# Kernel tuning notes

Hardware: AMD Instinct MI355X
Metric: run time of the kernel (lower is better)

## Reference

```python
import jax, jax.numpy as jnp
import numpy as np

EMB_SIZE = 256  # VQ embedding_size
BETA = 0.25     # commitment cost


def _mlp(x, W1, b1, W2, b2, W3, b3):
    h = jax.nn.relu(x @ W1 + b1)
    h = jax.nn.relu(h @ W2 + b2)
    return h @ W3 + b3


def setup_inputs() -> dict:
    key = jax.random.key(0)
    ks = jax.random.split(key, 5)
    B, D = 1024, 1024
    s = 1.0 / np.sqrt(D)
    return {
        "observation": jax.random.normal(ks[0], (B, D), jnp.float32),
        "W1": jax.random.normal(ks[1], (D, D), jnp.float32) * s,
        "b1": jnp.zeros((D,), jnp.float32),
        "W2": jax.random.normal(ks[2], (D, D), jnp.float32) * s,
        "b2": jnp.zeros((D,), jnp.float32),
        "W3": jax.random.normal(ks[3], (D, D), jnp.float32) * s,
        "b3": jnp.zeros((D,), jnp.float32),
        "codebook": jax.random.normal(ks[4], (512, EMB_SIZE), jnp.float32),
    }


def reference(observation, W1, b1, W2, b2, W3, b3, codebook):
    # Dense encoder
    features = _mlp(observation, W1, b1, W2, b2, W3, b3)  # [B, 1024]
    # Flatten features into embedding_size-dim tokens: [B*4, 256]
    z = features.reshape(-1, EMB_SIZE)
    # Squared euclidean distances to codebook: [N, K]
    d = (jnp.sum(z * z, axis=1, keepdims=True)
         - 2.0 * (z @ codebook.T)
         + jnp.sum(codebook * codebook, axis=1)[None, :])
    idx = jnp.argmin(d, axis=1)                   # [N] nearest code indices
    quantized = codebook[idx]                     # [N, 256] gather
    # VQ losses
    commitment_loss = jnp.mean((jax.lax.stop_gradient(quantized) - z) ** 2)
    codebook_loss = jnp.mean((quantized - jax.lax.stop_gradient(z)) ** 2)
    loss = codebook_loss + BETA * commitment_loss
    # Straight-through estimator
    quantized_st = z + jax.lax.stop_gradient(quantized - z)
    out = quantized_st.reshape(features.shape)    # [B, 1024]
    return out, loss, idx
```

## Files before the change

kernel.cpp:

```cpp
#include <hip/hip_runtime.h>


typedef _Float16 half8 __attribute__((ext_vector_type(8)));
typedef _Float16 half4 __attribute__((ext_vector_type(4)));
typedef float floatx4 __attribute__((ext_vector_type(4)));

#define LO_SCALE 2048.0f
#define INV_LO_SCALE (1.0f / 2048.0f)

__device__ __forceinline__ void write_granules(
    _Float16* __restrict__ lds, int row, int ks, int g0, int hh, half4 a, half4 b)
{
    const int sw = row & 7, base = row * 64;
    *reinterpret_cast<half4*>(&lds[base + (((ks * 4 + g0)    ) ^ sw) * 8 + hh * 4]) = a;
    *reinterpret_cast<half4*>(&lds[base + (((ks * 4 + g0 + 1)) ^ sw) * 8 + hh * 4]) = b;
}

__device__ __forceinline__ half8 read_frag(
    const _Float16* __restrict__ lds, int row, int ks, int g)
{
    const int gr = (ks * 4 + g) ^ (row & 7);
    return *reinterpret_cast<const half8*>(&lds[row * 64 + gr * 8]);
}

template <bool AF32, bool RELU, bool WF32, bool WSPLIT>
__global__ __launch_bounds__(512) void gemm_k(
    const float* __restrict__ Af,
    const _Float16* __restrict__ Ah, const _Float16* __restrict__ Al,
    const _Float16* __restrict__ Bh, const _Float16* __restrict__ Bl,
    const float* __restrict__ bias,
    float* __restrict__ Cf, _Float16* __restrict__ Ch, _Float16* __restrict__ Cl,
    int N, int K)
{
    __shared__ __align__(16) _Float16 sm[2][4][64 * 64];

    const int tid = threadIdx.x;
    const int m0 = blockIdx.y * 64, n0 = blockIdx.x * 64;

    const int so = tid & 7, srow = tid >> 3;
    const int ks_s = so >> 2, hh_s = (so >> 1) & 1, g0_s = (so & 1) * 2;
    const size_t aoff = (size_t)(m0 + srow) * K + so * 8;
    const size_t boff = (size_t)(n0 + srow) * K + so * 8;

    const int w = tid >> 6, l = tid & 63;
    const int wm = (w >> 2) * 32, wn = (w & 3) * 16;
    const int fr = l & 15, fg = l >> 4;

    float4 rA0, rA1;
    half8 rAh, rAl, rBh, rBl;

    auto LOAD = [&](int t) {
        const int kb = t * 64;
        if (AF32) {
            rA0 = *reinterpret_cast<const float4*>(&Af[aoff + kb]);
            rA1 = *reinterpret_cast<const float4*>(&Af[aoff + kb + 4]);
        } else {
            rAh = *reinterpret_cast<const half8*>(&Ah[aoff + kb]);
            rAl = *reinterpret_cast<const half8*>(&Al[aoff + kb]);
        }
        rBh = *reinterpret_cast<const half8*>(&Bh[boff + kb]);
        rBl = *reinterpret_cast<const half8*>(&Bl[boff + kb]);
    };

    auto WRITE = [&](int b) {
        half4 xa, xb;
        if (AF32) {
            float xs[8] = {rA0.x, rA0.y, rA0.z, rA0.w, rA1.x, rA1.y, rA1.z, rA1.w};
            half4 ha, hb, la, lb;
            #pragma unroll
            for (int j = 0; j < 4; ++j) {
                _Float16 hi = (_Float16)xs[j];
                ha[j] = hi; la[j] = (_Float16)((xs[j] - (float)hi) * LO_SCALE);
                hi = (_Float16)xs[4 + j];
                hb[j] = hi; lb[j] = (_Float16)((xs[4 + j] - (float)hi) * LO_SCALE);
            }
            write_granules(sm[b][0], srow, ks_s, g0_s, hh_s, ha, hb);
            write_granules(sm[b][1], srow, ks_s, g0_s, hh_s, la, lb);
        } else {
            #pragma unroll
            for (int j = 0; j < 4; ++j) { xa[j] = rAh[j]; xb[j] = rAh[j + 4]; }
            write_granules(sm[b][0], srow, ks_s, g0_s, hh_s, xa, xb);
            #pragma unroll
            for (int j = 0; j < 4; ++j) { xa[j] = rAl[j]; xb[j] = rAl[j + 4]; }
            write_granules(sm[b][1], srow, ks_s, g0_s, hh_s, xa, xb);
        }
        #pragma unroll
        for (int j = 0; j < 4; ++j) { xa[j] = rBh[j]; xb[j] = rBh[j + 4]; }
        write_granules(sm[b][2], srow, ks_s, g0_s, hh_s, xa, xb);
        #pragma unroll
        for (int j = 0; j < 4; ++j) { xa[j] = rBl[j]; xb[j] = rBl[j + 4]; }
        write_granules(sm[b][3], srow, ks_s, g0_s, hh_s, xa, xb);
    };

    floatx4 acc_hh[2] = {};
    floatx4 acc_mx[2] = {};

    const int NT = K >> 6;
    LOAD(0);
    WRITE(0);
    __syncthreads();

    for (int t = 0; t < NT; ++t) {
        const int cur = t & 1;
        if (t + 1 < NT) LOAD(t + 1);
        #pragma unroll
        for (int ks = 0; ks < 2; ++ks) {
            half8 a_h[2], a_l[2], b_h, b_l;
            #pragma unroll
            for (int i = 0; i < 2; ++i) {
                a_h[i] = read_frag(sm[cur][0], wm + i * 16 + fr, ks, fg);
                a_l[i] = read_frag(sm[cur][1], wm + i * 16 + fr, ks, fg);
            }
            b_h = read_frag(sm[cur][2], wn + fr, ks, fg);
            b_l = read_frag(sm[cur][3], wn + fr, ks, fg);
            #pragma unroll
            for (int i = 0; i < 2; ++i) {
                acc_hh[i] = __builtin_amdgcn_mfma_f32_16x16x32_f16(a_h[i], b_h, acc_hh[i], 0, 0, 0);
                acc_mx[i] = __builtin_amdgcn_mfma_f32_16x16x32_f16(a_h[i], b_l, acc_mx[i], 0, 0, 0);
                acc_mx[i] = __builtin_amdgcn_mfma_f32_16x16x32_f16(a_l[i], b_h, acc_mx[i], 0, 0, 0);
            }
        }
        if (t + 1 < NT) WRITE(cur ^ 1);
        __syncthreads();
    }

    const int col = n0 + wn + fr;
    const float bv = bias ? bias[col] : 0.0f;
    #pragma unroll
    for (int i = 0; i < 2; ++i) {
        #pragma unroll
        for (int r = 0; r < 4; ++r) {
            const int row = m0 + wm + i * 16 + fg * 4 + r;
            float v = acc_hh[i][r] + acc_mx[i][r] * INV_LO_SCALE + bv;
            if (RELU) v = fmaxf(v, 0.0f);
            const size_t o = (size_t)row * N + col;
            if (WF32) Cf[o] = v;
            if (WSPLIT) {
                const _Float16 hi = (_Float16)v;
                Ch[o] = hi;
                Cl[o] = (_Float16)((v - (float)hi) * LO_SCALE);
            }
        }
    }
}

__global__ __launch_bounds__(256) void splitT3_kernel(
    const float* __restrict__ W1, const float* __restrict__ W2, const float* __restrict__ W3,
    _Float16* __restrict__ T1h, _Float16* __restrict__ T1l,
    _Float16* __restrict__ T2h, _Float16* __restrict__ T2l,
    _Float16* __restrict__ T3h, _Float16* __restrict__ T3l)
{
    const int z = blockIdx.z;
    const float* Wm = (z == 0) ? W1 : (z == 1) ? W2 : W3;
    _Float16* Th = (z == 0) ? T1h : (z == 1) ? T2h : T3h;
    _Float16* Tl = (z == 0) ? T1l : (z == 1) ? T2l : T3l;

    __shared__ float tile[64][65];
    const int tid = threadIdx.x;
    const int kb = blockIdx.y * 64, nb = blockIdx.x * 64;
    {
        const int kr = tid >> 2, c0 = (tid & 3) * 16;
        #pragma unroll
        for (int c = 0; c < 16; c += 4) {
            float4 v = *reinterpret_cast<const float4*>(
                &Wm[(size_t)(kb + kr) * 1024 + nb + c0 + c]);
            tile[kr][c0 + c] = v.x; tile[kr][c0 + c + 1] = v.y;
            tile[kr][c0 + c + 2] = v.z; tile[kr][c0 + c + 3] = v.w;
        }
    }
    __syncthreads();
    {
        const int nr = tid >> 2, k0 = (tid & 3) * 16;
        half8 h[2], lo[2];
        #pragma unroll
        for (int c = 0; c < 16; ++c) {
            const float x = tile[k0 + c][nr];
            const _Float16 hi = (_Float16)x;
            h[c >> 3][c & 7] = hi;
            lo[c >> 3][c & 7] = (_Float16)((x - (float)hi) * LO_SCALE);
        }
        const size_t o = (size_t)(nb + nr) * 1024 + kb + k0;
        *reinterpret_cast<half8*>(&Th[o]) = h[0];
        *reinterpret_cast<half8*>(&Th[o + 8]) = h[1];
        *reinterpret_cast<half8*>(&Tl[o]) = lo[0];
        *reinterpret_cast<half8*>(&Tl[o + 8]) = lo[1];
    }
}

__global__ void cb_split_kernel(const float* __restrict__ CB,
                                _Float16* __restrict__ CBh, _Float16* __restrict__ CBl,
                                float* __restrict__ cnorm)
{
    const int k = blockIdx.x, lane = threadIdx.x;
    const int i = k * 256 + lane * 4;
    float4 c = *reinterpret_cast<const float4*>(&CB[i]);
    float xs[4] = {c.x, c.y, c.z, c.w};
    half4 h, lo;
    float s = 0.f;
    #pragma unroll
    for (int j = 0; j < 4; ++j) {
        const _Float16 hi = (_Float16)xs[j];
        h[j] = hi;
        lo[j] = (_Float16)((xs[j] - (float)hi) * LO_SCALE);
        s += xs[j] * xs[j];
    }
    *reinterpret_cast<half4*>(&CBh[i]) = h;
    *reinterpret_cast<half4*>(&CBl[i]) = lo;
    #pragma unroll
    for (int off = 32; off; off >>= 1) s += __shfl_down(s, off);
    if (lane == 0) cnorm[k] = s;
}

__global__ __launch_bounds__(512) void vq_kernel(
    const _Float16* __restrict__ Fh, const _Float16* __restrict__ Fl,
    const float* __restrict__ S, const float* __restrict__ CB,
    const float* __restrict__ cnorm,
    float* __restrict__ out, float* __restrict__ pl, float* __restrict__ idx_out)
{
    const int wid = threadIdx.x >> 6, lane = threadIdx.x & 63;
    const int n = blockIdx.x * 8 + wid;

    float best = 3.4e38f;
    int bidx = 0x7fffffff;
    #pragma unroll
    for (int j = 0; j < 8; ++j) {
        const int k = j * 64 + lane;
        const float v = fmaf(-2.0f, S[(size_t)n * 512 + k], cnorm[k]);
        if (v < best) { best = v; bidx = k; }
    }
    #pragma unroll
    for (int off = 32; off; off >>= 1) {
        const float ov = __shfl_down(best, off);
        const int oi = __shfl_down(bidx, off);
        if (ov < best || (ov == best && oi < bidx)) { best = ov; bidx = oi; }
    }
    bidx = __shfl(bidx, 0);
    best = __shfl(best, 0);

    const int base = n * 256 + lane * 4;
    half4 h4 = *reinterpret_cast<const half4*>(&Fh[base]);
    half4 l4 = *reinterpret_cast<const half4*>(&Fl[base]);
    float zn = 0.f;
    #pragma unroll
    for (int j = 0; j < 4; ++j) {
        const float z = (float)h4[j] + (float)l4[j] * INV_LO_SCALE;
        zn = fmaf(z, z, zn);
    }
    #pragma unroll
    for (int off = 32; off; off >>= 1) zn += __shfl_down(zn, off);

    float4 q4 = *reinterpret_cast<const float4*>(&CB[(size_t)bidx * 256 + lane * 4]);
    *reinterpret_cast<float4*>(&out[(size_t)n * 256 + lane * 4]) = q4;

    __shared__ float part[8];
    if (lane == 0) {
        part[wid] = zn + best;
        idx_out[n] = (float)bidx;
    }
    __syncthreads();
    if (threadIdx.x == 0) {
        float s = 0.f;
        #pragma unroll
        for (int i = 0; i < 8; ++i) s += part[i];
        pl[blockIdx.x] = s;
    }
}

__global__ __launch_bounds__(512) void finalize_kernel(
    const float* __restrict__ pl, float* __restrict__ loss_out)
{
    float s = pl[threadIdx.x];
    #pragma unroll
    for (int off = 32; off; off >>= 1) s += __shfl_down(s, off);
    __shared__ float p[8];
    if ((threadIdx.x & 63) == 0) p[threadIdx.x >> 6] = s;
    __syncthreads();
    if (threadIdx.x == 0) {
        float t = 0.f;
        #pragma unroll
        for (int i = 0; i < 8; ++i) t += p[i];
        loss_out[0] = 1.25f * t / 1048576.0f;
    }
}

extern "C" void kernel_launch(void* const* d_in, const int* in_sizes, int n_in,
                              void* d_out, int out_size, void* d_ws, size_t ws_size,
                              hipStream_t stream)
{
    const float* obs = (const float*)d_in[0];
    const float* W1  = (const float*)d_in[1];
    const float* b1  = (const float*)d_in[2];
    const float* W2  = (const float*)d_in[3];
    const float* b2  = (const float*)d_in[4];
    const float* W3  = (const float*)d_in[5];
    const float* b3  = (const float*)d_in[6];
    const float* CB  = (const float*)d_in[7];

    float* out = (float*)d_out;
    float* loss_out = out + 1048576;
    float* idx_out  = out + 1048577;

    char* Wp = (char*)d_ws;
    _Float16* W1t_h = (_Float16*)(Wp + (0u  << 20));
    _Float16* W1t_l = (_Float16*)(Wp + (2u  << 20));
    _Float16* W2t_h = (_Float16*)(Wp + (4u  << 20));
    _Float16* W2t_l = (_Float16*)(Wp + (6u  << 20));
    float*    S     = (float*)(Wp + (0u << 20));
    _Float16* W3t_h = (_Float16*)(Wp + (8u  << 20));
    _Float16* W3t_l = (_Float16*)(Wp + (10u << 20));
    _Float16* H1_h  = (_Float16*)(Wp + (12u << 20));
    _Float16* H1_l  = (_Float16*)(Wp + (14u << 20));
    _Float16* H2_h  = (_Float16*)(Wp + (16u << 20));
    _Float16* H2_l  = (_Float16*)(Wp + (18u << 20));
    _Float16* F_h   = (_Float16*)(Wp + (20u << 20));
    _Float16* F_l   = (_Float16*)(Wp + (22u << 20));
    _Float16* CB_h  = (_Float16*)(Wp + (24u << 20));
    _Float16* CB_l  = (_Float16*)(Wp + (24u << 20) + 512 * 256 * 2);
    float*    cn    = (float*)(Wp + (24u << 20) + 2 * 512 * 256 * 2);
    float*    pl    = cn + 512;

    splitT3_kernel<<<dim3(16, 16, 3), 256, 0, stream>>>(
        W1, W2, W3, W1t_h, W1t_l, W2t_h, W2t_l, W3t_h, W3t_l);
    cb_split_kernel<<<512, 64, 0, stream>>>(CB, CB_h, CB_l, cn);

    gemm_k<true, true, false, true><<<dim3(16, 16), 512, 0, stream>>>(
        obs, nullptr, nullptr, W1t_h, W1t_l, b1, nullptr, H1_h, H1_l, 1024, 1024);
    gemm_k<false, true, false, true><<<dim3(16, 16), 512, 0, stream>>>(
        nullptr, H1_h, H1_l, W2t_h, W2t_l, b2, nullptr, H2_h, H2_l, 1024, 1024);
    gemm_k<false, false, false, true><<<dim3(16, 16), 512, 0, stream>>>(
        nullptr, H2_h, H2_l, W3t_h, W3t_l, b3, nullptr, F_h, F_l, 1024, 1024);
    gemm_k<false, false, true, false><<<dim3(8, 64), 512, 0, stream>>>(
        nullptr, F_h, F_l, CB_h, CB_l, nullptr, S, nullptr, nullptr, 512, 256);

    vq_kernel<<<512, 512, 0, stream>>>(F_h, F_l, S, CB, cn, out, pl, idx_out);
    finalize_kernel<<<1, 512, 0, stream>>>(pl, loss_out);
}
```

Measured before the change: 137.2 us.

## Stage GEMM tiles with direct global-to-LDS loads and split-K across waves

Replaces the register-staged LDS writes in the split-fp16 GEMM with global_load_lds DMA copies, swizzling the global source address so no register round-trip is needed. The warp layout changes so the two k-halves of each 64-wide tile are computed by separate wave groups, each producing 32x32 outputs, and the partial sums are reduced through LDS in the epilogue. The observation fp32-to-hi/lo split moves into a separate prepass kernel so all GEMMs share one fp16 path. This trades an extra launch and extra workspace traffic, plus a reduction epilogue, for lower register pressure and less VALU work in the main loop.

```diff
diff --git a/kernel.cpp b/kernel.cpp
--- a/kernel.cpp
+++ b/kernel.cpp
@@ -8,24 +8,30 @@
 #define LO_SCALE 2048.0f
 #define INV_LO_SCALE (1.0f / 2048.0f)
 
-__device__ __forceinline__ void write_granules(
-    _Float16* __restrict__ lds, int row, int ks, int g0, int hh, half4 a, half4 b)
-{
-    const int sw = row & 7, base = row * 64;
-    *reinterpret_cast<half4*>(&lds[base + (((ks * 4 + g0)    ) ^ sw) * 8 + hh * 4]) = a;
-    *reinterpret_cast<half4*>(&lds[base + (((ks * 4 + g0 + 1)) ^ sw) * 8 + hh * 4]) = b;
-}
-
-__device__ __forceinline__ half8 read_frag(
-    const _Float16* __restrict__ lds, int row, int ks, int g)
-{
-    const int gr = (ks * 4 + g) ^ (row & 7);
-    return *reinterpret_cast<const half8*>(&lds[row * 64 + gr * 8]);
-}
-
-template <bool AF32, bool RELU, bool WF32, bool WSPLIT>
+__device__ __forceinline__ void gl_lds16(const _Float16* g, _Float16* l)
+{
+    __builtin_amdgcn_global_load_lds(
+        (const __attribute__((address_space(1))) void*)g,
+        (__attribute__((address_space(3))) void*)l, 16, 0, 0);
+}
+
+__device__ __forceinline__ half8 rfrag(const _Float16* m, int row, int ks, int fg)
+{
+    const int sw = row & 7;
+    const int c1 = ((ks << 2) + (fg >> 1)) ^ sw;
+    const int c2 = ((ks << 2) + (fg >> 1) + 2) ^ sw;
+    const int hs = (fg & 1) << 2;
+    const int rb = row << 6;
+    half4 x = *reinterpret_cast<const half4*>(&m[rb + (c1 << 3) + hs]);
+    half4 y = *reinterpret_cast<const half4*>(&m[rb + (c2 << 3) + hs]);
+    half8 r;
+    r[0] = x[0]; r[1] = x[1]; r[2] = x[2]; r[3] = x[3];
+    r[4] = y[0]; r[5] = y[1]; r[6] = y[2]; r[7] = y[3];
+    return r;
+}
+
+template <bool RELU, bool WF32, bool WSPLIT>
 __global__ __launch_bounds__(512) void gemm_k(
-    const float* __restrict__ Af,
     const _Float16* __restrict__ Ah, const _Float16* __restrict__ Al,
     const _Float16* __restrict__ Bh, const _Float16* __restrict__ Bl,
     const float* __restrict__ bias,
@@ -36,112 +42,114 @@
 
     const int tid = threadIdx.x;
     const int m0 = blockIdx.y * 64, n0 = blockIdx.x * 64;
-
-    const int so = tid & 7, srow = tid >> 3;
-    const int ks_s = so >> 2, hh_s = (so >> 1) & 1, g0_s = (so & 1) * 2;
-    const size_t aoff = (size_t)(m0 + srow) * K + so * 8;
-    const size_t boff = (size_t)(n0 + srow) * K + so * 8;
-
-    const int w = tid >> 6, l = tid & 63;
-    const int wm = (w >> 2) * 32, wn = (w & 3) * 16;
-    const int fr = l & 15, fg = l >> 4;
-
-    float4 rA0, rA1;
-    half8 rAh, rAl, rBh, rBl;
-
-    auto LOAD = [&](int t) {
-        const int kb = t * 64;
-        if (AF32) {
-            rA0 = *reinterpret_cast<const float4*>(&Af[aoff + kb]);
-            rA1 = *reinterpret_cast<const float4*>(&Af[aoff + kb + 4]);
-        } else {
-            rAh = *reinterpret_cast<const half8*>(&Ah[aoff + kb]);
-            rAl = *reinterpret_cast<const half8*>(&Al[aoff + kb]);
-        }
-        rBh = *reinterpret_cast<const half8*>(&Bh[boff + kb]);
-        rBl = *reinterpret_cast<const half8*>(&Bl[boff + kb]);
+    const int w = tid >> 6, lane = tid & 63;
+
+    const int mat = w >> 1;
+    const int half32 = (w & 1) * 32;
+    const _Float16* gsrc = (mat == 0) ? Ah : (mat == 1) ? Al : (mat == 2) ? Bh : Bl;
+    const int rb0 = (mat < 2) ? m0 : n0;
+    const int srow_lo = lane >> 3;
+    const int sc = lane & 7;
+
+    const int ks = w >> 2, q = w & 3;
+    const int wm = (q >> 1) * 32, wn = (q & 1) * 32;
+    const int fr = lane & 15, fg = lane >> 4;
+
+    floatx4 hh[2][2] = {};
+    floatx4 mx[2][2] = {};
+
+    const int NT = K >> 6;
+
+    auto STAGE = [&](int buf, int t) {
+        const int kb = t << 6;
+        #pragma unroll
+        for (int j = 0; j < 4; ++j) {
+            const int row = half32 + (j << 3) + srow_lo;
+            const _Float16* g = gsrc + (size_t)(rb0 + row) * K + kb
+                              + ((sc ^ (row & 7)) << 3);
+            gl_lds16(g, &sm[buf][mat][(half32 + (j << 3)) << 6]);
+        }
     };
 
-    auto WRITE = [&](int b) {
-        half4 xa, xb;
-        if (AF32) {
-            float xs[8] = {rA0.x, rA0.y, rA0.z, rA0.w, rA1.x, rA1.y, rA1.z, rA1.w};
-            half4 ha, hb, la, lb;
-            #pragma unroll
-            for (int j = 0; j < 4; ++j) {
-                _Float16 hi = (_Float16)xs[j];
-                ha[j] = hi; la[j] = (_Float16)((xs[j] - (float)hi) * LO_SCALE);
-                hi = (_Float16)xs[4 + j];
-                hb[j] = hi; lb[j] = (_Float16)((xs[4 + j] - (float)hi) * LO_SCALE);
-            }
-            write_granules(sm[b][0], srow, ks_s, g0_s, hh_s, ha, hb);
-            write_granules(sm[b][1], srow, ks_s, g0_s, hh_s, la, lb);
-        } else {
-            #pragma unroll
-            for (int j = 0; j < 4; ++j) { xa[j] = rAh[j]; xb[j] = rAh[j + 4]; }
-            write_granules(sm[b][0], srow, ks_s, g0_s, hh_s, xa, xb);
-            #pragma unroll
-            for (int j = 0; j < 4; ++j) { xa[j] = rAl[j]; xb[j] = rAl[j + 4]; }
-            write_granules(sm[b][1], srow, ks_s, g0_s, hh_s, xa, xb);
-        }
-        #pragma unroll
-        for (int j = 0; j < 4; ++j) { xa[j] = rBh[j]; xb[j] = rBh[j + 4]; }
-        write_granules(sm[b][2], srow, ks_s, g0_s, hh_s, xa, xb);
-        #pragma unroll
-        for (int j = 0; j < 4; ++j) { xa[j] = rBl[j]; xb[j] = rBl[j + 4]; }
-        write_granules(sm[b][3], srow, ks_s, g0_s, hh_s, xa, xb);
-    };
-
-    floatx4 acc_hh[2] = {};
-    floatx4 acc_mx[2] = {};
-
-    const int NT = K >> 6;
-    LOAD(0);
-    WRITE(0);
+    STAGE(0, 0);
     __syncthreads();
 
     for (int t = 0; t < NT; ++t) {
         const int cur = t & 1;
-        if (t + 1 < NT) LOAD(t + 1);
-        #pragma unroll
-        for (int ks = 0; ks < 2; ++ks) {
-            half8 a_h[2], a_l[2], b_h, b_l;
+        if (t + 1 < NT) STAGE(cur ^ 1, t + 1);
+
+        half8 a_h[2], a_l[2], b_h[2], b_l[2];
+        #pragma unroll
+        for (int i = 0; i < 2; ++i) {
+            a_h[i] = rfrag(sm[cur][0], wm + (i << 4) + fr, ks, fg);
+            a_l[i] = rfrag(sm[cur][1], wm + (i << 4) + fr, ks, fg);
+            b_h[i] = rfrag(sm[cur][2], wn + (i << 4) + fr, ks, fg);
+            b_l[i] = rfrag(sm[cur][3], wn + (i << 4) + fr, ks, fg);
+        }
+        #pragma unroll
+        for (int i = 0; i < 2; ++i)
             #pragma unroll
-            for (int i = 0; i < 2; ++i) {
-                a_h[i] = read_frag(sm[cur][0], wm + i * 16 + fr, ks, fg);
-                a_l[i] = read_frag(sm[cur][1], wm + i * 16 + fr, ks, fg);
+            for (int j = 0; j < 2; ++j) {
+                hh[i][j] = __builtin_amdgcn_mfma_f32_16x16x32_f16(a_h[i], b_h[j], hh[i][j], 0, 0, 0);
+                mx[i][j] = __builtin_amdgcn_mfma_f32_16x16x32_f16(a_h[i], b_l[j], mx[i][j], 0, 0, 0);
+                mx[i][j] = __builtin_amdgcn_mfma_f32_16x16x32_f16(a_l[i], b_h[j], mx[i][j], 0, 0, 0);
             }
-            b_h = read_frag(sm[cur][2], wn + fr, ks, fg);
-            b_l = read_frag(sm[cur][3], wn + fr, ks, fg);
+        __syncthreads();
+    }
+
+    float* red = (float*)&sm[0][0][0];
+    if (w >= 4) {
+        #pragma unroll
+        for (int i = 0; i < 2; ++i)
             #pragma unroll
-            for (int i = 0; i < 2; ++i) {
-                acc_hh[i] = __builtin_amdgcn_mfma_f32_16x16x32_f16(a_h[i], b_h, acc_hh[i], 0, 0, 0);
-                acc_mx[i] = __builtin_amdgcn_mfma_f32_16x16x32_f16(a_h[i], b_l, acc_mx[i], 0, 0, 0);
-                acc_mx[i] = __builtin_amdgcn_mfma_f32_16x16x32_f16(a_l[i], b_h, acc_mx[i], 0, 0, 0);
-            }
-        }
-        if (t + 1 < NT) WRITE(cur ^ 1);
-        __syncthreads();
-    }
-
-    const int col = n0 + wn + fr;
-    const float bv = bias ? bias[col] : 0.0f;
-    #pragma unroll
-    for (int i = 0; i < 2; ++i) {
-        #pragma unroll
-        for (int r = 0; r < 4; ++r) {
-            const int row = m0 + wm + i * 16 + fg * 4 + r;
-            float v = acc_hh[i][r] + acc_mx[i][r] * INV_LO_SCALE + bv;
-            if (RELU) v = fmaxf(v, 0.0f);
-            const size_t o = (size_t)row * N + col;
-            if (WF32) Cf[o] = v;
-            if (WSPLIT) {
-                const _Float16 hi = (_Float16)v;
-                Ch[o] = hi;
-                Cl[o] = (_Float16)((v - (float)hi) * LO_SCALE);
-            }
-        }
-    }
+            for (int j = 0; j < 2; ++j)
+                #pragma unroll
+                for (int r = 0; r < 4; ++r)
+                    red[q * 1024 + ((i << 4) + (fg << 2) + r) * 32 + (j << 4) + fr]
+                        = hh[i][j][r] + mx[i][j][r] * INV_LO_SCALE;
+    }
+    __syncthreads();
+    if (w < 4) {
+        #pragma unroll
+        for (int j = 0; j < 2; ++j) {
+            const int col = n0 + wn + (j << 4) + fr;
+            const float bv = bias ? bias[col] : 0.0f;
+            #pragma unroll
+            for (int i = 0; i < 2; ++i)
+                #pragma unroll
+                for (int r = 0; r < 4; ++r) {
+                    const int rl = (i << 4) + (fg << 2) + r;
+                    float v = hh[i][j][r] + mx[i][j][r] * INV_LO_SCALE
+                            + red[q * 1024 + rl * 32 + (j << 4) + fr] + bv;
+                    if (RELU) v = fmaxf(v, 0.0f);
+                    const size_t o = (size_t)(m0 + wm + rl) * N + col;
+                    if (WF32) Cf[o] = v;
+                    if (WSPLIT) {
+                        const _Float16 hi = (_Float16)v;
+                        Ch[o] = hi;
+                        Cl[o] = (_Float16)((v - (float)hi) * LO_SCALE);
+                    }
+                }
+        }
+    }
+}
+
+__global__ __launch_bounds__(256) void split_kernel(
+    const float* __restrict__ X, _Float16* __restrict__ H, _Float16* __restrict__ L)
+{
+    const int i = (blockIdx.x * 256 + threadIdx.x) * 8;
+    float4 a = *reinterpret_cast<const float4*>(&X[i]);
+    float4 b = *reinterpret_cast<const float4*>(&X[i + 4]);
+    float xs[8] = {a.x, a.y, a.z, a.w, b.x, b.y, b.z, b.w};
+    half8 h, lo;
+    #pragma unroll
+    for (int j = 0; j < 8; ++j) {
+        const _Float16 hi = (_Float16)xs[j];
+        h[j] = hi;
+        lo[j] = (_Float16)((xs[j] - (float)hi) * LO_SCALE);
+    }
+    *reinterpret_cast<half8*>(&H[i]) = h;
+    *reinterpret_cast<half8*>(&L[i]) = lo;
 }
 
 __global__ __launch_bounds__(256) void splitT3_kernel(
@@ -301,36 +309,39 @@
     float* idx_out  = out + 1048577;
 
     char* Wp = (char*)d_ws;
-    _Float16* W1t_h = (_Float16*)(Wp + (0u  << 20));
-    _Float16* W1t_l = (_Float16*)(Wp + (2u  << 20));
-    _Float16* W2t_h = (_Float16*)(Wp + (4u  << 20));
-    _Float16* W2t_l = (_Float16*)(Wp + (6u  << 20));
-    float*    S     = (float*)(Wp + (0u << 20));
-    _Float16* W3t_h = (_Float16*)(Wp + (8u  << 20));
-    _Float16* W3t_l = (_Float16*)(Wp + (10u << 20));
-    _Float16* H1_h  = (_Float16*)(Wp + (12u << 20));
-    _Float16* H1_l  = (_Float16*)(Wp + (14u << 20));
-    _Float16* H2_h  = (_Float16*)(Wp + (16u << 20));
-    _Float16* H2_l  = (_Float16*)(Wp + (18u << 20));
-    _Float16* F_h   = (_Float16*)(Wp + (20u << 20));
-    _Float16* F_l   = (_Float16*)(Wp + (22u << 20));
-    _Float16* CB_h  = (_Float16*)(Wp + (24u << 20));
-    _Float16* CB_l  = (_Float16*)(Wp + (24u << 20) + 512 * 256 * 2);
-    float*    cn    = (float*)(Wp + (24u << 20) + 2 * 512 * 256 * 2);
+    _Float16* Oh    = (_Float16*)(Wp + (0u  << 20));
+    _Float16* Ol    = (_Float16*)(Wp + (2u  << 20));
+    _Float16* W1t_h = (_Float16*)(Wp + (4u  << 20));
+    _Float16* W1t_l = (_Float16*)(Wp + (6u  << 20));
+    _Float16* W2t_h = (_Float16*)(Wp + (8u  << 20));
+    _Float16* W2t_l = (_Float16*)(Wp + (10u << 20));
+    _Float16* W3t_h = (_Float16*)(Wp + (12u << 20));
+    _Float16* W3t_l = (_Float16*)(Wp + (14u << 20));
+    _Float16* H1_h  = (_Float16*)(Wp + (16u << 20));
+    _Float16* H1_l  = (_Float16*)(Wp + (18u << 20));
+    _Float16* H2_h  = (_Float16*)(Wp + (20u << 20));
+    _Float16* H2_l  = (_Float16*)(Wp + (22u << 20));
+    _Float16* F_h   = (_Float16*)(Wp + (24u << 20));
+    _Float16* F_l   = (_Float16*)(Wp + (26u << 20));
+    float*    S     = (float*)(Wp + (28u << 20));
+    _Float16* CB_h  = (_Float16*)(Wp + (36u << 20));
+    _Float16* CB_l  = (_Float16*)(Wp + (36u << 20) + 512 * 256 * 2);
+    float*    cn    = (float*)(Wp + (36u << 20) + 2 * 512 * 256 * 2);
     float*    pl    = cn + 512;
 
+    split_kernel<<<512, 256, 0, stream>>>(obs, Oh, Ol);
     splitT3_kernel<<<dim3(16, 16, 3), 256, 0, stream>>>(
         W1, W2, W3, W1t_h, W1t_l, W2t_h, W2t_l, W3t_h, W3t_l);
     cb_split_kernel<<<512, 64, 0, stream>>>(CB, CB_h, CB_l, cn);
 
-    gemm_k<true, true, false, true><<<dim3(16, 16), 512, 0, stream>>>(
-        obs, nullptr, nullptr, W1t_h, W1t_l, b1, nullptr, H1_h, H1_l, 1024, 1024);
-    gemm_k<false, true, false, true><<<dim3(16, 16), 512, 0, stream>>>(
-        nullptr, H1_h, H1_l, W2t_h, W2t_l, b2, nullptr, H2_h, H2_l, 1024, 1024);
-    gemm_k<false, false, false, true><<<dim3(16, 16), 512, 0, stream>>>(
-        nullptr, H2_h, H2_l, W3t_h, W3t_l, b3, nullptr, F_h, F_l, 1024, 1024);
-    gemm_k<false, false, true, false><<<dim3(8, 64), 512, 0, stream>>>(
-        nullptr, F_h, F_l, CB_h, CB_l, nullptr, S, nullptr, nullptr, 512, 256);
+    gemm_k<true, false, true><<<dim3(16, 16), 512, 0, stream>>>(
+        Oh, Ol, W1t_h, W1t_l, b1, nullptr, H1_h, H1_l, 1024, 1024);
+    gemm_k<true, false, true><<<dim3(16, 16), 512, 0, stream>>>(
+        H1_h, H1_l, W2t_h, W2t_l, b2, nullptr, H2_h, H2_l, 1024, 1024);
+    gemm_k<false, false, true><<<dim3(16, 16), 512, 0, stream>>>(
+        H2_h, H2_l, W3t_h, W3t_l, b3, nullptr, F_h, F_l, 1024, 1024);
+    gemm_k<false, true, false><<<dim3(8, 64), 512, 0, stream>>>(
+        F_h, F_l, CB_h, CB_l, nullptr, S, nullptr, nullptr, 512, 256);
 
     vq_kernel<<<512, 512, 0, stream>>>(F_h, F_l, S, CB, cn, out, pl, idx_out);
     finalize_kernel<<<1, 512, 0, stream>>>(pl, loss_out);
```

New measurement: 147.6 us. 1.08x slower.
